# Optimization experiments

Hardware: AMD Instinct MI355X
Metric: run time of the kernel (lower is better)

The kernel has to match this reference:

```python
import jax, jax.numpy as jnp
import numpy as np

INVALID = 1e9  # distance value marking a missing arc (>= 1e6 threshold in source)
TEMPERATURE = 0.5


def setup_inputs() -> dict:
    n = 4096
    key = jax.random.key(0)
    k_d, k_m, k_l = jax.random.split(key, 3)
    dist = jax.random.uniform(k_d, (n, n), dtype=jnp.float32, minval=0.0, maxval=100.0)
    keep = jax.random.uniform(k_m, (n, n)) < 0.5
    distance_matrix = jnp.where(keep, dist, INVALID).astype(jnp.float32)
    logits = (-2.0 + 0.5 * jax.random.normal(k_l, (n, n))).astype(jnp.float32)
    attention_logits = jnp.zeros((n, n), dtype=jnp.float32)
    return {
        "distance_matrix": distance_matrix,
        "logits": logits,
        "attention_logits": attention_logits,
        "source": 0,
        "destination": n - 1,
    }


def reference(distance_matrix, logits, attention_logits, source, destination):
    n = distance_matrix.shape[0]
    valid = (distance_matrix < 1e6).astype(jnp.float32)
    density = jnp.sum(valid) / (n * n)
    mu1 = 1.0
    mu2 = 10.0 * (1.0 + density)
    mu3 = 10.0 * (1.0 + density)

    # decision matrix (dense branch)
    attention = jax.nn.softmax(attention_logits, axis=1)
    x = jax.nn.sigmoid(logits / TEMPERATURE) * attention * valid  # [n, n]

    # flow penalty: vectorized form of the per-node loop
    out_flow = jnp.sum(x, axis=1)  # [n]
    in_flow = jnp.sum(x, axis=0)   # [n]
    d = out_flow - in_flow
    d = d.at[source].add(-1.0).at[destination].add(1.0)
    flow_penalty = jnp.sum(d * d)

    path_cost = jnp.sum(distance_matrix * x)  # invalid arcs have x == 0
    binary_penalty = jnp.sum(x * (1.0 - x))

    # connectivity: 10-step matmul power iteration (min(n-1, 10) = 10 for n > 11)
    reach = x
    for _ in range(10):
        reach = jnp.minimum(reach + reach @ x, 1.0)
    connectivity_penalty = jnp.square(1.0 - reach[source, destination])

    sparsity_penalty = jnp.sum(x) / (n * n)
    n_edges = jnp.sum(valid)

    return (mu1 * path_cost / (n_edges + 1e-6)
            + mu2 * flow_penalty / n
            + mu3 * binary_penalty / (n * n)
            + 20.0 * connectivity_penalty
            + 5.0 * sparsity_penalty)
```

## Files before the change

kernel.cpp:

```cpp
#include <hip/hip_runtime.h>
#include <hip/hip_bf16.h>
#include <cmath>

typedef unsigned short u16;
typedef unsigned int u32;

__device__ __forceinline__ float bf2f(u16 b) {
    return __uint_as_float(((u32)b) << 16);
}
__device__ __forceinline__ u16 f2bf(float f) {
    u32 u = __float_as_uint(f);
    u = (u + 0x7fffu + ((u >> 16) & 1u)) >> 16;
    return (u16)u;
}

__device__ __forceinline__ float wave_sum(float v) {
#pragma unroll
    for (int o = 32; o > 0; o >>= 1) v += __shfl_xor(v, o, 64);
    return v;
}

__device__ float block_sum(float v) {
    __shared__ float s[4];
    v = wave_sum(v);
    __syncthreads();
    if ((threadIdx.x & 63) == 0) s[threadIdx.x >> 6] = v;
    __syncthreads();
    return s[0] + s[1] + s[2] + s[3];
}

template <int K>
__global__ __launch_bounds__(256) void k_x(
    const float* __restrict__ dist, const float* __restrict__ logit,
    const float* __restrict__ attn, const int* __restrict__ srcp,
    u16* __restrict__ xb, float* __restrict__ pp, float* __restrict__ v,
    int n, int nbx) {
    const int bx = blockIdx.x;
    const int row = blockIdx.y;
    const int t = threadIdx.x;
    const int lane = t & 63;
    const int wv = t >> 6;
    const size_t base = (size_t)row * n;
    const int c0 = bx * 1024 * K;

    float4 a4[K], d4[K], l4[K];
#pragma unroll
    for (int k = 0; k < K; ++k) {
        const int col = c0 + 4 * t + 1024 * k;
        a4[k] = *(const float4*)(attn + base + col);
        d4[k] = *(const float4*)(dist + base + col);
        l4[k] = *(const float4*)(logit + base + col);
    }
    const int src = *srcp;

    float se = 0.f, cnt = 0.f, s1 = 0.f, s2 = 0.f, pc = 0.f;
#pragma unroll
    for (int k = 0; k < K; ++k) {
        const int col = c0 + 4 * t + 1024 * k;
        const float ev[4] = {__expf(a4[k].x), __expf(a4[k].y),
                             __expf(a4[k].z), __expf(a4[k].w)};
        const float dv[4] = {d4[k].x, d4[k].y, d4[k].z, d4[k].w};
        const float lv[4] = {l4[k].x, l4[k].y, l4[k].z, l4[k].w};
        float yv[4];
        ushort4 pk;
        u16* pkp = (u16*)&pk;
#pragma unroll
        for (int q = 0; q < 4; ++q) {
            float valid = (dv[q] < 1.0e6f) ? 1.f : 0.f;
            float sg = 1.0f / (1.0f + __expf(-2.0f * lv[q]));
            float y = sg * ev[q] * valid;
            yv[q] = y;
            se += ev[q];
            cnt += valid;
            s1 += y;
            s2 += y * y;
            pc += dv[q] * y;
            pkp[q] = f2bf(y);
        }
        *(ushort4*)(xb + base + col) = pk;
        if (row == src) {
            float4 vf; vf.x = yv[0]; vf.y = yv[1]; vf.z = yv[2]; vf.w = yv[3];
            *(float4*)(v + col) = vf;
        }
    }

    se = wave_sum(se);
    cnt = wave_sum(cnt);
    s1 = wave_sum(s1);
    s2 = wave_sum(s2);
    pc = wave_sum(pc);
    __shared__ float red[4][5];
    if (lane == 0) {
        red[wv][0] = se; red[wv][1] = cnt; red[wv][2] = s1;
        red[wv][3] = s2; red[wv][4] = pc;
    }
    __syncthreads();
    if (t == 0) {
        const size_t nb = (size_t)nbx * n;
        const size_t idx = (size_t)bx * n + row;
        pp[0 * nb + idx] = red[0][0] + red[1][0] + red[2][0] + red[3][0];
        pp[1 * nb + idx] = red[0][1] + red[1][1] + red[2][1] + red[3][1];
        pp[2 * nb + idx] = red[0][2] + red[1][2] + red[2][2] + red[3][2];
        pp[3 * nb + idx] = red[0][3] + red[1][3] + red[2][3] + red[3][3];
        pp[4 * nb + idx] = red[0][4] + red[1][4] + red[2][4] + red[3][4];
    }
}

__global__ __launch_bounds__(256) void k_z(
    const float* __restrict__ pp, float* __restrict__ izrow,
    float* __restrict__ out_flow, float* __restrict__ cnt_row,
    float* __restrict__ s2_row, float* __restrict__ pc_row, int n, int nbx) {
    const int j = blockIdx.x * 256 + threadIdx.x;
    const size_t nb = (size_t)nbx * n;
    float SE = 0.f, CN = 0.f, S1 = 0.f, S2 = 0.f, PC = 0.f;
    for (int c = 0; c < nbx; ++c) {
        const size_t idx = (size_t)c * n + j;
        SE += pp[0 * nb + idx];
        CN += pp[1 * nb + idx];
        S1 += pp[2 * nb + idx];
        S2 += pp[3 * nb + idx];
        PC += pp[4 * nb + idx];
    }
    const float iz = 1.0f / SE;
    izrow[j] = iz;
    out_flow[j] = S1 * iz;
    cnt_row[j] = CN;
    s2_row[j] = S2 * iz * iz;
    pc_row[j] = PC * iz;
}

template <int FIRST>
__global__ __launch_bounds__(256) void k_iter(
    const u16* __restrict__ xb, const float* __restrict__ v_in,
    const float* __restrict__ up_in, float* __restrict__ v_out,
    float* __restrict__ up_out, float* __restrict__ ip,
    const float* __restrict__ izrow, const int* __restrict__ srcp,
    int n, int nbx, int rc) {
    __shared__ float vl[64];
    __shared__ float wz[64];
    __shared__ float vparts[4][64];
    const int t = threadIdx.x;
    const int lin = blockIdx.x;
    const int xcd = lin & 7;
    const int slot = lin >> 3;
    const int bx = slot % nbx;
    const int by = xcd * ((gridDim.x >> 3) / nbx) + slot / nbx;
    const int rows_per = n / rc;
    const int i0 = by * rows_per;
    const int j0 = bx * 1024 + t * 4;

    if (FIRST) {
        if (t < rows_per) {
            const float iz_src = izrow[*srcp];
            const float a = v_in[i0 + t] * iz_src;
            const float iz = izrow[i0 + t];
            vl[t] = a * iz;
            wz[t] = iz;
            if (bx == 0) v_out[i0 + t] = a;
        }
    } else {
        const int i = t & 63, g = t >> 6;
        const int cpg = rc >> 2;
        float a = 0.f;
#pragma unroll 4
        for (int c = g * cpg; c < (g + 1) * cpg; ++c)
            a += up_in[(size_t)c * n + i0 + i];
        vparts[g][i] = a;
        __syncthreads();
        if (t < rows_per) {
            const float s = v_in[i0 + t] + vparts[0][t] + vparts[1][t] +
                            vparts[2][t] + vparts[3][t];
            vl[t] = s * izrow[i0 + t];
            if (bx == 0) v_out[i0 + t] = s;
        }
    }
    __syncthreads();

    float4 acc = {0.f, 0.f, 0.f, 0.f};
    float4 cs = {0.f, 0.f, 0.f, 0.f};
#pragma unroll 8
    for (int i = 0; i < rows_per; ++i) {
        ushort4 xv = *(const ushort4*)(xb + (size_t)(i0 + i) * n + j0);
        float vi = vl[i];
        acc.x = fmaf(vi, bf2f(xv.x), acc.x);
        acc.y = fmaf(vi, bf2f(xv.y), acc.y);
        acc.z = fmaf(vi, bf2f(xv.z), acc.z);
        acc.w = fmaf(vi, bf2f(xv.w), acc.w);
        if (FIRST) {
            float wi = wz[i];
            cs.x = fmaf(wi, bf2f(xv.x), cs.x);
            cs.y = fmaf(wi, bf2f(xv.y), cs.y);
            cs.z = fmaf(wi, bf2f(xv.z), cs.z);
            cs.w = fmaf(wi, bf2f(xv.w), cs.w);
        }
    }
    *(float4*)(up_out + (size_t)by * n + j0) = acc;
    if (FIRST) *(float4*)(ip + (size_t)by * n + j0) = cs;
}

__global__ __launch_bounds__(256) void k_reduce(
    const float* __restrict__ out_flow, const float* __restrict__ ip,
    const float* __restrict__ cnt_row, const float* __restrict__ s2_row,
    const float* __restrict__ pc_row, const int* __restrict__ srcp,
    const int* __restrict__ dstp, float* __restrict__ pb, int n, int nchunk) {
    const int t = threadIdx.x;
    const int j = blockIdx.x * 256 + t;
    const int src = *srcp, dst = *dstp;
    float infl = 0.f;
#pragma unroll 8
    for (int c = 0; c < nchunk; ++c) infl += ip[(size_t)c * n + j];
    float d = out_flow[j] - infl;
    if (j == src) d -= 1.f;
    if (j == dst) d += 1.f;
    float f = block_sum(d * d);
    float s1 = block_sum(out_flow[j]);
    float cnt = block_sum(cnt_row[j]);
    float s2 = block_sum(s2_row[j]);
    float pc = block_sum(pc_row[j]);
    if (t == 0) {
        float* p = pb + blockIdx.x * 5;
        p[0] = f; p[1] = s1; p[2] = cnt; p[3] = s2; p[4] = pc;
    }
}

__global__ __launch_bounds__(256) void k_final(
    const float* __restrict__ pb, const float* __restrict__ v_last,
    const float* __restrict__ up_last, const int* __restrict__ dstp,
    float* __restrict__ out, int n, int nblk, int nchunk) {
    const int t = threadIdx.x;
    const int dst = *dstp;
    float flow = block_sum(t < nblk ? pb[t * 5 + 0] : 0.f);
    float S1   = block_sum(t < nblk ? pb[t * 5 + 1] : 0.f);
    float NE   = block_sum(t < nblk ? pb[t * 5 + 2] : 0.f);
    float S2   = block_sum(t < nblk ? pb[t * 5 + 3] : 0.f);
    float PC   = block_sum(t < nblk ? pb[t * 5 + 4] : 0.f);
    float r = block_sum(t < nchunk ? up_last[(size_t)t * n + dst] : 0.f);
    if (t == 0) {
        r += v_last[dst];
        float nf = (float)n;
        float nn = nf * nf;
        float density = NE / nn;
        float mu2 = 10.f * (1.f + density);
        float om = 1.f - r;
        float res = PC / (NE + 1e-6f)
                  + mu2 * flow / nf
                  + mu2 * (S1 - S2) / nn
                  + 20.f * om * om
                  + 5.f * S1 / nn;
        out[0] = res;
    }
}

extern "C" void kernel_launch(void* const* d_in, const int* in_sizes, int n_in,
                              void* d_out, int out_size, void* d_ws, size_t ws_size,
                              hipStream_t stream) {
    const float* dist = (const float*)d_in[0];
    const float* logit = (const float*)d_in[1];
    const float* attn = (const float*)d_in[2];
    const int* srcp = (const int*)d_in[3];
    const int* dstp = (const int*)d_in[4];
    const int n = (int)(std::sqrt((double)in_sizes[0]) + 0.5);
    const size_t nn = (size_t)n * n;

    const int RC = 64;
    const int nbx = n / 1024;

    const int KX = (n >= 2048) ? 2 : 1;
    const int xbx = n / (1024 * KX);

    char* ws = (char*)d_ws;
    u16* xb = (u16*)ws;
    float* f = (float*)(ws + nn * sizeof(u16));
    float* out_flow = f; f += n;
    float* cnt_row = f;  f += n;
    float* s2_row = f;   f += n;
    float* pc_row = f;   f += n;
    float* vA = f;       f += n;
    float* vB = f;       f += n;
    float* izrow = f;    f += n;
    float* pp = f;       f += (size_t)5 * xbx * n;
    float* upA = f;      f += (size_t)RC * n;
    float* upB = f;      f += (size_t)RC * n;
    float* ip = f;       f += (size_t)RC * n;
    float* pb = f;       f += 128;

    if (KX == 2)
        k_x<2><<<dim3(xbx, n), 256, 0, stream>>>(dist, logit, attn, srcp, xb,
                                                 pp, vA, n, xbx);
    else
        k_x<1><<<dim3(xbx, n), 256, 0, stream>>>(dist, logit, attn, srcp, xb,
                                                 pp, vA, n, xbx);

    k_z<<<n / 256, 256, 0, stream>>>(pp, izrow, out_flow, cnt_row, s2_row,
                                     pc_row, n, xbx);

    const int niblk = nbx * RC;

    k_iter<1><<<niblk, 256, 0, stream>>>(xb, vA, nullptr, vB, upA, ip,
                                         izrow, srcp, n, nbx, RC);
    float* vin = vB;  float* uin = upA;
    float* vout;      float* uout;
    for (int it = 2; it <= 10; ++it) {
        vout = (it & 1) ? vB : vA;
        uout = (it & 1) ? upA : upB;
        k_iter<0><<<niblk, 256, 0, stream>>>(xb, vin, uin, vout, uout, nullptr,
                                             izrow, srcp, n, nbx, RC);
        vin = vout; uin = uout;
    }

    k_reduce<<<n / 256, 256, 0, stream>>>(out_flow, ip, cnt_row, s2_row,
                                          pc_row, srcp, dstp, pb, n, RC);
    k_final<<<1, 256, 0, stream>>>(pb, vin, uin, dstp, (float*)d_out, n,
                                   n / 256, RC);
}
```

Baseline: 118.6 us.

## Meet-in-the-middle reachability: iterate forward and backward vectors five steps each

Replaces the ten sequential vector-matrix iterations from the source row with five iterations that advance both a forward row vector (source) and a backward column vector (destination) in the same pass over the bf16 matrix. The final reach value comes from the dot product of the two half-length vectors, computed in the reduce kernel. This halves the number of full matrix sweeps and kernel launches. The cost is extra per-row wave reductions and shared-memory traffic inside each iteration. It also relies on the clamp-free linear recurrence being splittable, which the prior code already assumed.

```diff
diff --git a/kernel.cpp b/kernel.cpp
--- a/kernel.cpp
+++ b/kernel.cpp
@@ -130,113 +130,147 @@
 }
 
 template <int FIRST>
-__global__ __launch_bounds__(256) void k_iter(
-    const u16* __restrict__ xb, const float* __restrict__ v_in,
-    const float* __restrict__ up_in, float* __restrict__ v_out,
-    float* __restrict__ up_out, float* __restrict__ ip,
-    const float* __restrict__ izrow, const int* __restrict__ srcp,
-    int n, int nbx, int rc) {
-    __shared__ float vl[64];
-    __shared__ float wz[64];
-    __shared__ float vparts[4][64];
+__global__ __launch_bounds__(256) void k_it(
+    const u16* __restrict__ xb,
+    const float* __restrict__ u_in, const float* __restrict__ ufp_in,
+    const float* __restrict__ w_in, const float* __restrict__ wfp_in,
+    float* __restrict__ u_out, float* __restrict__ ufp_out,
+    float* __restrict__ w_out, float* __restrict__ wfp_out,
+    float* __restrict__ ip, const float* __restrict__ izrow,
+    const int* __restrict__ srcp, const int* __restrict__ dstp,
+    int n, int nbx) {
+    __shared__ float vl[64], wz[64], wl[1024];
+    __shared__ float vparts[4][64], bwp[4][64];
     const int t = threadIdx.x;
+    const int lane = t & 63, wv = t >> 6;
     const int lin = blockIdx.x;
-    const int xcd = lin & 7;
-    const int slot = lin >> 3;
+    const int xcd = lin & 7, slot = lin >> 3;
     const int bx = slot % nbx;
     const int by = xcd * ((gridDim.x >> 3) / nbx) + slot / nbx;
-    const int rows_per = n / rc;
-    const int i0 = by * rows_per;
-    const int j0 = bx * 1024 + t * 4;
+    const int i0 = by * 64;
+    const int j0 = bx * 1024;
 
     if (FIRST) {
-        if (t < rows_per) {
-            const float iz_src = izrow[*srcp];
-            const float a = v_in[i0 + t] * iz_src;
-            const float iz = izrow[i0 + t];
-            vl[t] = a * iz;
-            wz[t] = iz;
-            if (bx == 0) v_out[i0 + t] = a;
+        if (t < 64) {
+            const float izs = izrow[*srcp];
+            const float u0 = u_in[i0 + t] * izs;
+            vl[t] = u0 * izrow[i0 + t];
+            wz[t] = izrow[i0 + t];
+            if (bx == 0) u_out[i0 + t] = u0;
         }
     } else {
         const int i = t & 63, g = t >> 6;
-        const int cpg = rc >> 2;
         float a = 0.f;
 #pragma unroll 4
-        for (int c = g * cpg; c < (g + 1) * cpg; ++c)
-            a += up_in[(size_t)c * n + i0 + i];
+        for (int c = g * 16; c < (g + 1) * 16; ++c)
+            a += ufp_in[(size_t)c * n + i0 + i];
         vparts[g][i] = a;
         __syncthreads();
-        if (t < rows_per) {
-            const float s = v_in[i0 + t] + vparts[0][t] + vparts[1][t] +
+        if (t < 64) {
+            const float s = u_in[i0 + t] + vparts[0][t] + vparts[1][t] +
                             vparts[2][t] + vparts[3][t];
             vl[t] = s * izrow[i0 + t];
-            if (bx == 0) v_out[i0 + t] = s;
-        }
-    }
-    __syncthreads();
+            if (bx == 0) u_out[i0 + t] = s;
+        }
+    }
+
+    const int dst = *dstp;
+#pragma unroll
+    for (int kk = 0; kk < 4; ++kk) {
+        const int jj = j0 + kk * 256 + t;
+        float wvv;
+        if (FIRST) {
+            wvv = (jj == dst) ? 1.f : 0.f;
+        } else {
+            float s = 0.f;
+            for (int c = 0; c < nbx; ++c) s += wfp_in[(size_t)c * n + jj];
+            wvv = w_in[jj] + izrow[jj] * s;
+        }
+        wl[kk * 256 + t] = wvv;
+        if (by == 0) w_out[jj] = wvv;
+    }
+    __syncthreads();
+
+    const float wr0 = wl[4 * t + 0], wr1 = wl[4 * t + 1];
+    const float wr2 = wl[4 * t + 2], wr3 = wl[4 * t + 3];
+    const int jcol = j0 + 4 * t;
 
     float4 acc = {0.f, 0.f, 0.f, 0.f};
     float4 cs = {0.f, 0.f, 0.f, 0.f};
-#pragma unroll 8
-    for (int i = 0; i < rows_per; ++i) {
-        ushort4 xv = *(const ushort4*)(xb + (size_t)(i0 + i) * n + j0);
-        float vi = vl[i];
-        acc.x = fmaf(vi, bf2f(xv.x), acc.x);
-        acc.y = fmaf(vi, bf2f(xv.y), acc.y);
-        acc.z = fmaf(vi, bf2f(xv.z), acc.z);
-        acc.w = fmaf(vi, bf2f(xv.w), acc.w);
+#pragma unroll 4
+    for (int i = 0; i < 64; ++i) {
+        const ushort4 xv = *(const ushort4*)(xb + (size_t)(i0 + i) * n + jcol);
+        const float x0 = bf2f(xv.x), x1 = bf2f(xv.y);
+        const float x2 = bf2f(xv.z), x3 = bf2f(xv.w);
+        const float vi = vl[i];
+        acc.x = fmaf(vi, x0, acc.x);
+        acc.y = fmaf(vi, x1, acc.y);
+        acc.z = fmaf(vi, x2, acc.z);
+        acc.w = fmaf(vi, x3, acc.w);
         if (FIRST) {
-            float wi = wz[i];
-            cs.x = fmaf(wi, bf2f(xv.x), cs.x);
-            cs.y = fmaf(wi, bf2f(xv.y), cs.y);
-            cs.z = fmaf(wi, bf2f(xv.z), cs.z);
-            cs.w = fmaf(wi, bf2f(xv.w), cs.w);
-        }
-    }
-    *(float4*)(up_out + (size_t)by * n + j0) = acc;
-    if (FIRST) *(float4*)(ip + (size_t)by * n + j0) = cs;
+            const float wi = wz[i];
+            cs.x = fmaf(wi, x0, cs.x);
+            cs.y = fmaf(wi, x1, cs.y);
+            cs.z = fmaf(wi, x2, cs.z);
+            cs.w = fmaf(wi, x3, cs.w);
+        }
+        float b = fmaf(x0, wr0, fmaf(x1, wr1, fmaf(x2, wr2, x3 * wr3)));
+        b = wave_sum(b);
+        if (lane == 0) bwp[wv][i] = b;
+    }
+    *(float4*)(ufp_out + (size_t)by * n + jcol) = acc;
+    if (FIRST) *(float4*)(ip + (size_t)by * n + jcol) = cs;
+    __syncthreads();
+    if (t < 64)
+        wfp_out[(size_t)bx * n + i0 + t] =
+            bwp[0][t] + bwp[1][t] + bwp[2][t] + bwp[3][t];
 }
 
 __global__ __launch_bounds__(256) void k_reduce(
     const float* __restrict__ out_flow, const float* __restrict__ ip,
     const float* __restrict__ cnt_row, const float* __restrict__ s2_row,
-    const float* __restrict__ pc_row, const int* __restrict__ srcp,
-    const int* __restrict__ dstp, float* __restrict__ pb, int n, int nchunk) {
+    const float* __restrict__ pc_row, const float* __restrict__ u_in,
+    const float* __restrict__ ufp, const float* __restrict__ w_in,
+    const float* __restrict__ wfp, const float* __restrict__ izrow,
+    const int* __restrict__ srcp, const int* __restrict__ dstp,
+    float* __restrict__ pb, int n, int nbx) {
     const int t = threadIdx.x;
     const int j = blockIdx.x * 256 + t;
     const int src = *srcp, dst = *dstp;
     float infl = 0.f;
 #pragma unroll 8
-    for (int c = 0; c < nchunk; ++c) infl += ip[(size_t)c * n + j];
+    for (int c = 0; c < 64; ++c) infl += ip[(size_t)c * n + j];
     float d = out_flow[j] - infl;
     if (j == src) d -= 1.f;
     if (j == dst) d += 1.f;
+    float u5 = u_in[j];
+#pragma unroll 8
+    for (int c = 0; c < 64; ++c) u5 += ufp[(size_t)c * n + j];
+    float ws = 0.f;
+    for (int c = 0; c < nbx; ++c) ws += wfp[(size_t)c * n + j];
+    const float w5 = w_in[j] + izrow[j] * ws;
     float f = block_sum(d * d);
     float s1 = block_sum(out_flow[j]);
     float cnt = block_sum(cnt_row[j]);
     float s2 = block_sum(s2_row[j]);
     float pc = block_sum(pc_row[j]);
+    float dot = block_sum(u5 * w5);
     if (t == 0) {
-        float* p = pb + blockIdx.x * 5;
-        p[0] = f; p[1] = s1; p[2] = cnt; p[3] = s2; p[4] = pc;
+        float* p = pb + blockIdx.x * 6;
+        p[0] = f; p[1] = s1; p[2] = cnt; p[3] = s2; p[4] = pc; p[5] = dot;
     }
 }
 
 __global__ __launch_bounds__(256) void k_final(
-    const float* __restrict__ pb, const float* __restrict__ v_last,
-    const float* __restrict__ up_last, const int* __restrict__ dstp,
-    float* __restrict__ out, int n, int nblk, int nchunk) {
+    const float* __restrict__ pb, float* __restrict__ out, int n, int nblk) {
     const int t = threadIdx.x;
-    const int dst = *dstp;
-    float flow = block_sum(t < nblk ? pb[t * 5 + 0] : 0.f);
-    float S1   = block_sum(t < nblk ? pb[t * 5 + 1] : 0.f);
-    float NE   = block_sum(t < nblk ? pb[t * 5 + 2] : 0.f);
-    float S2   = block_sum(t < nblk ? pb[t * 5 + 3] : 0.f);
-    float PC   = block_sum(t < nblk ? pb[t * 5 + 4] : 0.f);
-    float r = block_sum(t < nchunk ? up_last[(size_t)t * n + dst] : 0.f);
+    float flow = block_sum(t < nblk ? pb[t * 6 + 0] : 0.f);
+    float S1   = block_sum(t < nblk ? pb[t * 6 + 1] : 0.f);
+    float NE   = block_sum(t < nblk ? pb[t * 6 + 2] : 0.f);
+    float S2   = block_sum(t < nblk ? pb[t * 6 + 3] : 0.f);
+    float PC   = block_sum(t < nblk ? pb[t * 6 + 4] : 0.f);
+    float r    = block_sum(t < nblk ? pb[t * 6 + 5] : 0.f);
     if (t == 0) {
-        r += v_last[dst];
         float nf = (float)n;
         float nn = nf * nf;
         float density = NE / nn;
@@ -262,9 +296,7 @@
     const int n = (int)(std::sqrt((double)in_sizes[0]) + 0.5);
     const size_t nn = (size_t)n * n;
 
-    const int RC = 64;
     const int nbx = n / 1024;
-
     const int KX = (n >= 2048) ? 2 : 1;
     const int xbx = n / (1024 * KX);
 
@@ -276,12 +308,17 @@
     float* s2_row = f;   f += n;
     float* pc_row = f;   f += n;
     float* vA = f;       f += n;
-    float* vB = f;       f += n;
     float* izrow = f;    f += n;
+    float* ubA = f;      f += n;
+    float* ubB = f;      f += n;
+    float* wbA = f;      f += n;
+    float* wbB = f;      f += n;
+    float* ip = f;       f += (size_t)64 * n;
+    float* ufpA = f;     f += (size_t)64 * n;
+    float* ufpB = f;     f += (size_t)64 * n;
+    float* wfpA = f;     f += (size_t)4 * n;
+    float* wfpB = f;     f += (size_t)4 * n;
     float* pp = f;       f += (size_t)5 * xbx * n;
-    float* upA = f;      f += (size_t)RC * n;
-    float* upB = f;      f += (size_t)RC * n;
-    float* ip = f;       f += (size_t)RC * n;
     float* pb = f;       f += 128;
 
     if (KX == 2)
@@ -294,22 +331,24 @@
     k_z<<<n / 256, 256, 0, stream>>>(pp, izrow, out_flow, cnt_row, s2_row,
                                      pc_row, n, xbx);
 
-    const int niblk = nbx * RC;
-
-    k_iter<1><<<niblk, 256, 0, stream>>>(xb, vA, nullptr, vB, upA, ip,
-                                         izrow, srcp, n, nbx, RC);
-    float* vin = vB;  float* uin = upA;
-    float* vout;      float* uout;
-    for (int it = 2; it <= 10; ++it) {
-        vout = (it & 1) ? vB : vA;
-        uout = (it & 1) ? upA : upB;
-        k_iter<0><<<niblk, 256, 0, stream>>>(xb, vin, uin, vout, uout, nullptr,
-                                             izrow, srcp, n, nbx, RC);
-        vin = vout; uin = uout;
+    const int niblk = nbx * 64;
+
+    k_it<1><<<niblk, 256, 0, stream>>>(xb, vA, nullptr, nullptr, nullptr,
+                                       ubA, ufpA, wbA, wfpA, ip,
+                                       izrow, srcp, dstp, n, nbx);
+    for (int it = 2; it <= 5; ++it) {
+        const bool even = (it & 1) == 0;
+        float* ui = even ? ubA : ubB;   float* uo = even ? ubB : ubA;
+        float* fi = even ? ufpA : ufpB; float* fo = even ? ufpB : ufpA;
+        float* wi = even ? wbA : wbB;   float* wo = even ? wbB : wbA;
+        float* gi = even ? wfpA : wfpB; float* go = even ? wfpB : wfpA;
+        k_it<0><<<niblk, 256, 0, stream>>>(xb, ui, fi, wi, gi,
+                                           uo, fo, wo, go, nullptr,
+                                           izrow, srcp, dstp, n, nbx);
     }
 
     k_reduce<<<n / 256, 256, 0, stream>>>(out_flow, ip, cnt_row, s2_row,
-                                          pc_row, srcp, dstp, pb, n, RC);
-    k_final<<<1, 256, 0, stream>>>(pb, vin, uin, dstp, (float*)d_out, n,
-                                   n / 256, RC);
-}
+                                          pc_row, ubA, ufpA, wbA, wfpA,
+                                          izrow, srcp, dstp, pb, n, nbx);
+    k_final<<<1, 256, 0, stream>>>(pb, (float*)d_out, n, n / 256);
+}
```

After: 230.6 us. 94.4% more time.
